# Kernel optimization log

Measured on AMD Instinct MI355X. Metric: run time of the kernel, lower is better.

## Reference

```python
import jax, jax.numpy as jnp
import numpy as np

B = 1024
M = 131072          # memory_size
K = 256             # key_dim
CHOOSE_K = 256
BETA = 1e-08
EPS = 0.001


def setup_inputs() -> dict:
    key = jax.random.key(0)
    k1, k2, k3 = jax.random.split(key, 3)
    q = jax.random.normal(k1, (B, K), dtype=jnp.float32)
    mk = jax.random.normal(k2, (M, K), dtype=jnp.float32)
    memory_key = mk / jnp.linalg.norm(mk, axis=1, keepdims=True)  # unit-norm keys as in update_memory
    # __init__: first half values = 1 (real), second half = 0 (fake)
    memory_values = jnp.concatenate([jnp.ones((M // 2,), jnp.float32),
                                     jnp.zeros((M - M // 2,), jnp.float32)])
    # hist starts near 1e-5; add small positive noise so p_c is non-degenerate
    memory_hist = 1e-05 + 1e-05 * jax.random.uniform(k3, (M,), dtype=jnp.float32)
    return {"q": q, "memory_key": memory_key,
            "memory_values": memory_values, "memory_hist": memory_hist}


def reference(q, memory_key, memory_values, memory_hist):
    # similarities: [B, M]
    similarities = jnp.matmul(q, memory_key.T)
    p_x_given_c_unnorm = jnp.exp(similarities)
    hist_b = memory_hist + BETA
    p_c = hist_b / jnp.sum(hist_b)                       # [M]
    p_c_given_x = p_x_given_c_unnorm * p_c               # [B, M]
    p_c_given_x_approx, idxs = jax.lax.top_k(p_c_given_x, CHOOSE_K)  # [B, k]
    vals = memory_values[idxs]                           # gather, [B, k]
    p_y_given_x_unnorm = jnp.sum(vals * p_c_given_x_approx, axis=1)
    p_y_given_x = p_y_given_x_unnorm / jnp.sum(p_c_given_x_approx, axis=1)
    return jnp.clip(p_y_given_x, EPS, 1.0 - EPS)
```

## Files before the change

kernel.cpp:

```cpp
#include <hip/hip_runtime.h>
#include <math.h>
#include <stdint.h>

#define MMEM 131072
#define KDIM 256
#define NB   1024
#define TOPK 256
#define BETA_F 1e-08f
#define NTILE 2048
#define OVFCAP 65536
#define SLOTS 4
#define SBINS 1024
#define SCAP  2560
#define SBCAP 256

typedef _Float16 f16x8 __attribute__((ext_vector_type(8)));
typedef float    f32x4 __attribute__((ext_vector_type(4)));

__device__ __forceinline__ void gload16(const void* g, void* l) {
  __builtin_amdgcn_global_load_lds(
      (const __attribute__((address_space(1))) uint32_t*)g,
      (__attribute__((address_space(3))) uint32_t*)l, 16, 0, 0);
}

#define NQ4 (NB * KDIM / 4)
#define NM4 (MMEM * KDIM / 4)
#define CVTB ((NQ4 + NM4) / 256)
__global__ __launch_bounds__(256) void prep_kernel(const float* __restrict__ q,
                                                   const float* __restrict__ mk,
                                                   _Float16* __restrict__ qh,
                                                   _Float16* __restrict__ mkh,
                                                   const float* __restrict__ hist,
                                                   float* __restrict__ partials,
                                                   float* __restrict__ partials_log) {
  const int b = blockIdx.x;
  if (b < CVTB) {
    int i = b * 256 + threadIdx.x;
    const float* in; _Float16* out; int j;
    if (i < NQ4) { in = q; out = qh; j = i; }
    else         { in = mk; out = mkh; j = i - NQ4; }
    float4 v = *(const float4*)&in[(size_t)j * 4];
    union { _Float16 h[4]; uint2 u; } p;
    p.h[0] = (_Float16)v.x; p.h[1] = (_Float16)v.y;
    p.h[2] = (_Float16)v.z; p.h[3] = (_Float16)v.w;
    *(uint2*)&out[(size_t)j * 4] = p.u;
    return;
  }
  const int bid = b - CVTB;
  float s = 0.f, sl = 0.f;
  for (int i = bid * 256 + threadIdx.x; i < MMEM; i += 256 * 256) {
    float h = hist[i] + BETA_F;
    s += h;
    sl += logf(h);
  }
  #pragma unroll
  for (int off = 32; off > 0; off >>= 1) {
    s  += __shfl_down(s, off);
    sl += __shfl_down(sl, off);
  }
  __shared__ float ws[4], wsl[4];
  int lane = threadIdx.x & 63, wid = threadIdx.x >> 6;
  if (lane == 0) { ws[wid] = s; wsl[wid] = sl; }
  __syncthreads();
  if (threadIdx.x == 0) {
    partials[bid]     = ws[0] + ws[1] + ws[2] + ws[3];
    partials_log[bid] = wsl[0] + wsl[1] + wsl[2] + wsl[3];
  }
}

__global__ __launch_bounds__(256) void logpc_final_kernel(const float* __restrict__ hist,
                                                          const float* __restrict__ partials,
                                                          const float* __restrict__ partials_log,
                                                          float* __restrict__ logpc,
                                                          float* __restrict__ out_sum,
                                                          float* __restrict__ out_thresh,
                                                          uint32_t* __restrict__ ovf_cnt,
                                                          float z0) {
  __shared__ float ws[4], wsl[4];
  const int tid = threadIdx.x;
  float s = partials[tid];
  float sl = (blockIdx.x == 0) ? partials_log[tid] : 0.f;
  #pragma unroll
  for (int off = 32; off > 0; off >>= 1) {
    s  += __shfl_down(s, off);
    sl += __shfl_down(sl, off);
  }
  int lane = tid & 63, wid = tid >> 6;
  if (lane == 0) { ws[wid] = s; wsl[wid] = sl; }
  __syncthreads();
  const float sum = ws[0] + ws[1] + ws[2] + ws[3];
  const int i = blockIdx.x * 256 + tid;
  logpc[i] = logf(hist[i] + BETA_F) - logf(sum);
  if (blockIdx.x == 0 && tid == 0) {
    float suml = wsl[0] + wsl[1] + wsl[2] + wsl[3];
    *out_sum = sum;
    *out_thresh = suml / (float)MMEM - logf(sum) + z0;
    *ovf_cnt = 0u;
  }
}

__global__ __launch_bounds__(256, 3) void gemm_kernel(const _Float16* __restrict__ qh,
                                                      const _Float16* __restrict__ mkh,
                                                      const float* __restrict__ logpc,
                                                      const float* __restrict__ values,
                                                      const float* __restrict__ thresh,
                                                      float2* __restrict__ cand,
                                                      uint8_t* __restrict__ cnt,
                                                      int4* __restrict__ ovf,
                                                      uint32_t* __restrict__ ovf_cnt) {
  __shared__ _Float16 As[3][4096];
  __shared__ _Float16 Bs[3][4096];

  const int t    = threadIdx.x;
  const int lane = t & 63;
  const int wave = t >> 6;
  const int wr   = (wave & 1) * 64;
  const int wc   = (wave >> 1) * 64;
  const int lm   = lane & 15;
  const int lk   = lane >> 4;

  const int wg  = blockIdx.x;
  const int lg  = ((wg & 7) << 10) | (wg >> 3);
  const int row0 = (lg & 7) << 7;
  const int col0 = (lg >> 3) << 7;

  const int r0q = t >> 2;
  const int cc  = (t & 3) ^ ((r0q >> 1) & 3);

  const char* gA0 = (const char*)qh  + ((size_t)(row0 + r0q)      * KDIM) * 2 + cc * 16;
  const char* gA1 = (const char*)qh  + ((size_t)(row0 + 64 + r0q) * KDIM) * 2 + cc * 16;
  const char* gB0 = (const char*)mkh + ((size_t)(col0 + r0q)      * KDIM) * 2 + cc * 16;
  const char* gB1 = (const char*)mkh + ((size_t)(col0 + 64 + r0q) * KDIM) * 2 + cc * 16;

  int offA[4], offB[4];
  #pragma unroll
  for (int i = 0; i < 4; ++i) {
    int ar = wr + i * 16 + lm;
    offA[i] = ar * 64 + ((lk ^ ((ar >> 1) & 3)) * 16);
    int br = wc + i * 16 + lm;
    offB[i] = br * 64 + ((lk ^ ((br >> 1) & 3)) * 16);
  }

  const float tv = *thresh;
  float lpv[4], vv[4];
  #pragma unroll
  for (int j = 0; j < 4; ++j) {
    lpv[j] = logpc[col0 + wc + j * 16 + lm];
    vv[j]  = values[col0 + wc + j * 16 + lm];
  }
  asm volatile("s_waitcnt vmcnt(0)" ::: "memory");

  f32x4 acc[4][4];
  #pragma unroll
  for (int i = 0; i < 4; i++)
    #pragma unroll
    for (int j = 0; j < 4; j++)
      acc[i][j] = (f32x4){0.f, 0.f, 0.f, 0.f};

  auto stage = [&](int buf, int chunk) {
    const size_t ko = (size_t)chunk * 64;
    gload16(gA0 + ko, (char*)&As[buf][0] + t * 16);
    gload16(gA1 + ko, (char*)&As[buf][0] + 4096 + t * 16);
    gload16(gB0 + ko, (char*)&Bs[buf][0] + t * 16);
    gload16(gB1 + ko, (char*)&Bs[buf][0] + 4096 + t * 16);
  };

  stage(0, 0);
  stage(1, 1);
  asm volatile("s_waitcnt vmcnt(4)" ::: "memory");
  __builtin_amdgcn_s_barrier();
  asm volatile("" ::: "memory");

  #pragma unroll
  for (int it = 0; it < 8; ++it) {
    const int cur = it % 3;
    const char* Ab = (const char*)&As[cur][0];
    const char* Bb = (const char*)&Bs[cur][0];
    f16x8 af[4], bf[4];
    #pragma unroll
    for (int i = 0; i < 4; ++i) af[i] = *(const f16x8*)(Ab + offA[i]);
    #pragma unroll
    for (int j = 0; j < 4; ++j) bf[j] = *(const f16x8*)(Bb + offB[j]);
    if (it + 2 < 8) stage((it + 2) % 3, it + 2);
    __builtin_amdgcn_s_setprio(1);
    #pragma unroll
    for (int i = 0; i < 4; ++i)
      #pragma unroll
      for (int j = 0; j < 4; ++j)
        acc[i][j] = __builtin_amdgcn_mfma_f32_16x16x32_f16(af[i], bf[j], acc[i][j], 0, 0, 0);
    __builtin_amdgcn_s_setprio(0);
    if (it < 7) {
      if (it + 2 < 8) asm volatile("s_waitcnt vmcnt(4)" ::: "memory");
      else            asm volatile("s_waitcnt vmcnt(0)" ::: "memory");
      __builtin_amdgcn_s_barrier();
      asm volatile("" ::: "memory");
    }
  }

  const int coltile = (col0 + wc) >> 6;
  const uint32_t ltm = (1u << lm) - 1u;
  const int shift = lane & 48;
  #pragma unroll
  for (int i = 0; i < 4; ++i) {
    #pragma unroll
    for (int r4 = 0; r4 < 4; ++r4) {
      const int row = row0 + wr + i * 16 + lk * 4 + r4;
      float sv[4];
      uint32_t gm[4];
      int tot = 0;
      #pragma unroll
      for (int j = 0; j < 4; ++j) {
        sv[j] = acc[i][j][r4] + lpv[j];
        gm[j] = (uint32_t)((__ballot(sv[j] >= tv) >> shift) & 0xFFFFull);
        tot += __popc(gm[j]);
      }
      const size_t bucket = (size_t)row * NTILE + coltile;
      if (lm == 0) cnt[bucket] = (uint8_t)(tot < SLOTS ? tot : SLOTS);
      float2* bs = cand + bucket * SLOTS;
      int prev = 0;
      #pragma unroll
      for (int j = 0; j < 4; ++j) {
        if ((gm[j] >> lm) & 1u) {
          int k = prev + __popc(gm[j] & ltm);
          if (k < SLOTS) {
            bs[k] = make_float2(sv[j], vv[j]);
          } else {
            int col = col0 + wc + j * 16 + lm;
            uint32_t p = atomicAdd(ovf_cnt, 1u);
            if (p < OVFCAP) ovf[p] = make_int4(row, col, __float_as_int(sv[j]),
                                               __float_as_int(vv[j]));
          }
        }
        prev += __popc(gm[j]);
      }
    }
  }
}

__global__ __launch_bounds__(512) void select_kernel(const float2* __restrict__ cand,
                                                     const uint8_t* __restrict__ cnt,
                                                     const int4* __restrict__ ovf,
                                                     const uint32_t* __restrict__ ovf_cnt,
                                                     const float* __restrict__ thresh,
                                                     float* __restrict__ out) {
  __shared__ uint32_t hist[SBINS];
  __shared__ float cs_s[SCAP];
  __shared__ float cs_v[SCAP];
  __shared__ uint32_t csum[32];
  __shared__ int s_bstar, s_above, s_ccnt, s_bcnt;
  __shared__ float bin_s[SBCAP];
  __shared__ float bin_v[SBCAP];
  __shared__ float red_p[8], red_vp[8];

  const int tid = threadIdx.x;
  const int row = blockIdx.x;
  const float tv = *thresh;
  const int novf = (int)min(*ovf_cnt, (uint32_t)OVFCAP);

  for (int i = tid; i < SBINS; i += 512) hist[i] = 0;
  if (tid == 0) { s_ccnt = 0; s_bcnt = 0; }
  __syncthreads();

  for (int tile = tid; tile < NTILE; tile += 512) {
    size_t bucket = (size_t)row * NTILE + tile;
    int c = (int)cnt[bucket];
    if (c > 0) {
      const float4* b4 = (const float4*)(cand + bucket * SLOTS);
      float4 lo = b4[0];
      float4 hi = b4[1];
      float sc0 = lo.x, vl0 = lo.y, sc1 = lo.z, vl1 = lo.w;
      float sc2 = hi.x, vl2 = hi.y, sc3 = hi.z, vl3 = hi.w;
      #pragma unroll
      for (int k = 0; k < 4; k++) {
        if (k < c) {
          float s = (k == 0) ? sc0 : (k == 1) ? sc1 : (k == 2) ? sc2 : sc3;
          float v = (k == 0) ? vl0 : (k == 1) ? vl1 : (k == 2) ? vl2 : vl3;
          int b = (int)((s - tv) * 256.0f);
          b = b < 0 ? 0 : (b > SBINS - 1 ? SBINS - 1 : b);
          atomicAdd(&hist[b], 1u);
          int pos = atomicAdd(&s_ccnt, 1);
          if (pos < SCAP) { cs_s[pos] = s; cs_v[pos] = v; }
        }
      }
    }
  }
  for (int i = tid; i < novf; i += 512) {
    int4 e = ovf[i];
    if (e.x == row) {
      float s = __int_as_float(e.z);
      float v = __int_as_float(e.w);
      int b = (int)((s - tv) * 256.0f);
      b = b < 0 ? 0 : (b > SBINS - 1 ? SBINS - 1 : b);
      atomicAdd(&hist[b], 1u);
      int pos = atomicAdd(&s_ccnt, 1);
      if (pos < SCAP) { cs_s[pos] = s; cs_v[pos] = v; }
    }
  }
  __syncthreads();

  if (tid < 32) {
    uint32_t s = 0;
    for (int b = 0; b < 32; b++) s += hist[tid * 32 + b];
    csum[tid] = s;
  }
  __syncthreads();
  if (tid == 0) {
    uint32_t cum = 0;
    int bstar = 0; uint32_t above = 0;
    for (int c = 31; c >= 0; c--) {
      if (cum + csum[c] >= TOPK) {
        for (int b = 31; b >= 0; b--) {
          uint32_t h = hist[c * 32 + b];
          if (cum + h >= TOPK) { bstar = c * 32 + b; above = cum; goto found; }
          cum += h;
        }
      }
      cum += csum[c];
    }
    bstar = 0; above = cum - hist[0];
  found:
    s_bstar = bstar;
    s_above = (int)above;
  }
  __syncthreads();
  const int bstar = s_bstar;
  int rneed = TOPK - s_above;
  const int ctot = s_ccnt;

  float psum = 0.f, vpsum = 0.f;
  if (ctot <= SCAP) {
    for (int i = tid; i < ctot; i += 512) {
      float s = cs_s[i];
      float v = cs_v[i];
      int b = (int)((s - tv) * 256.0f);
      b = b < 0 ? 0 : (b > SBINS - 1 ? SBINS - 1 : b);
      if (b > bstar) {
        float p = __expf(s);
        psum += p;
        vpsum += p * v;
      } else if (b == bstar) {
        int pos = atomicAdd(&s_bcnt, 1);
        if (pos < SBCAP) { bin_s[pos] = s; bin_v[pos] = v; }
      }
    }
  } else {
    for (int tile = tid; tile < NTILE; tile += 512) {
      size_t bucket = (size_t)row * NTILE + tile;
      int c = (int)cnt[bucket];
      const float2* bs = cand + bucket * SLOTS;
      for (int k = 0; k < c; k++) {
        float2 e = bs[k];
        int b = (int)((e.x - tv) * 256.0f);
        b = b < 0 ? 0 : (b > SBINS - 1 ? SBINS - 1 : b);
        if (b > bstar) {
          float p = __expf(e.x);
          psum += p;
          vpsum += p * e.y;
        } else if (b == bstar) {
          int pos = atomicAdd(&s_bcnt, 1);
          if (pos < SBCAP) { bin_s[pos] = e.x; bin_v[pos] = e.y; }
        }
      }
    }
    for (int i = tid; i < novf; i += 512) {
      int4 e = ovf[i];
      if (e.x == row) {
        float s = __int_as_float(e.z);
        float v = __int_as_float(e.w);
        int b = (int)((s - tv) * 256.0f);
        b = b < 0 ? 0 : (b > SBINS - 1 ? SBINS - 1 : b);
        if (b > bstar) {
          float p = __expf(s);
          psum += p;
          vpsum += p * v;
        } else if (b == bstar) {
          int pos = atomicAdd(&s_bcnt, 1);
          if (pos < SBCAP) { bin_s[pos] = s; bin_v[pos] = v; }
        }
      }
    }
  }
  __syncthreads();

  int c2 = s_bcnt < SBCAP ? s_bcnt : SBCAP;
  int n2 = 1;
  while (n2 < c2) n2 <<= 1;
  for (int i = c2 + tid; i < n2; i += 512) { bin_s[i] = -INFINITY; bin_v[i] = 0.f; }
  __syncthreads();

  for (int size = 2; size <= n2; size <<= 1) {
    for (int stride = size >> 1; stride > 0; stride >>= 1) {
      for (int i = tid; i < n2; i += 512) {
        int j = i ^ stride;
        if (j > i) {
          float si = bin_s[i], sj = bin_s[j];
          float vi = bin_v[i], vj = bin_v[j];
          bool igt = (si > sj) || (si == sj && vi > vj);
          bool desc = ((i & size) == 0);
          if (desc ? !igt : igt) {
            bin_s[i] = sj; bin_s[j] = si;
            bin_v[i] = vj; bin_v[j] = vi;
          }
        }
      }
      __syncthreads();
    }
  }

  int take = rneed < c2 ? rneed : c2;
  if (take < 0) take = 0;
  for (int i = tid; i < take; i += 512) {
    float p = __expf(bin_s[i]);
    psum += p;
    vpsum += p * bin_v[i];
  }

  #pragma unroll
  for (int off = 32; off > 0; off >>= 1) {
    psum  += __shfl_down(psum, off);
    vpsum += __shfl_down(vpsum, off);
  }
  int lane = tid & 63, wid = tid >> 6;
  if (lane == 0) { red_p[wid] = psum; red_vp[wid] = vpsum; }
  __syncthreads();
  if (tid == 0) {
    float P = 0.f, V = 0.f;
    for (int w = 0; w < 8; w++) { P += red_p[w]; V += red_vp[w]; }
    float r = V / P;
    r = fminf(fmaxf(r, 1e-3f), 1.0f - 1e-3f);
    out[row] = r;
  }
}

extern "C" void kernel_launch(void* const* d_in, const int* in_sizes, int n_in,
                              void* d_out, int out_size, void* d_ws, size_t ws_size,
                              hipStream_t stream) {
  const float* q      = (const float*)d_in[0];
  const float* mk     = (const float*)d_in[1];
  const float* values = (const float*)d_in[2];
  const float* hist   = (const float*)d_in[3];
  float* out = (float*)d_out;

  float*    ws_sum   = (float*)d_ws;
  float*    ws_thr   = (float*)((char*)d_ws + 64);
  uint32_t* ovf_cnt  = (uint32_t*)((char*)d_ws + 128);
  float*    partials = (float*)((char*)d_ws + 4096);
  float*    partialsl= (float*)((char*)d_ws + 8192);
  float*    logpc    = (float*)((char*)d_ws + 16384);
  _Float16* qh       = (_Float16*)((char*)d_ws + 540672);
  _Float16* mkh      = (_Float16*)((char*)d_ws + 1064960);
  uint8_t*  cnt      = (uint8_t*)((char*)d_ws + 68173824ull);
  int4*     ovf      = (int4*)((char*)d_ws + 76562432ull);
  float2*   cand     = (float2*)((char*)d_ws + 77611008ull);

  const float z0 = 2.4176f;

  prep_kernel<<<CVTB + 256, 256, 0, stream>>>(q, mk, qh, mkh, hist, partials, partialsl);
  logpc_final_kernel<<<MMEM / 256, 256, 0, stream>>>(hist, partials, partialsl, logpc,
                                                     ws_sum, ws_thr, ovf_cnt, z0);
  gemm_kernel<<<(NB / 128) * (MMEM / 128), 256, 0, stream>>>(
      qh, mkh, logpc, values, ws_thr, cand, cnt, ovf, ovf_cnt);
  select_kernel<<<NB, 512, 0, stream>>>(cand, cnt, ovf, ovf_cnt, ws_thr, out);
}
```

Measured before the change: 340.3 us.

## Widen fp16 conversion, skip empty bucket writes, scan counts by word, split GEMM launch

The fp16 conversion in prep now has each thread handle 16 floats with 128-bit stores instead of 4 floats per thread. In the GEMM epilogue, lanes skip the candidate-store loop when a bucket has no hits. The select kernel reads the per-tile counts four bytes at a time and skips all-zero words. The GEMM launch is also split into two half-grid launches using a workgroup offset, which adds one launch but leaves total work the same.

```diff
diff --git a/kernel.cpp b/kernel.cpp
--- a/kernel.cpp
+++ b/kernel.cpp
@@ -23,9 +23,9 @@
       (__attribute__((address_space(3))) uint32_t*)l, 16, 0, 0);
 }
 
-#define NQ4 (NB * KDIM / 4)
-#define NM4 (MMEM * KDIM / 4)
-#define CVTB ((NQ4 + NM4) / 256)
+#define NQ16 (NB * KDIM / 16)
+#define NM16 (MMEM * KDIM / 16)
+#define CVTB ((NQ16 + NM16) / 256)
 __global__ __launch_bounds__(256) void prep_kernel(const float* __restrict__ q,
                                                    const float* __restrict__ mk,
                                                    _Float16* __restrict__ qh,
@@ -36,14 +36,20 @@
   const int b = blockIdx.x;
   if (b < CVTB) {
     int i = b * 256 + threadIdx.x;
-    const float* in; _Float16* out; int j;
-    if (i < NQ4) { in = q; out = qh; j = i; }
-    else         { in = mk; out = mkh; j = i - NQ4; }
-    float4 v = *(const float4*)&in[(size_t)j * 4];
-    union { _Float16 h[4]; uint2 u; } p;
-    p.h[0] = (_Float16)v.x; p.h[1] = (_Float16)v.y;
-    p.h[2] = (_Float16)v.z; p.h[3] = (_Float16)v.w;
-    *(uint2*)&out[(size_t)j * 4] = p.u;
+    const float* in; _Float16* out; size_t j;
+    if (i < NQ16) { in = q;  out = qh;  j = (size_t)i; }
+    else          { in = mk; out = mkh; j = (size_t)(i - NQ16); }
+    const float4* src = (const float4*)(in + j * 16);
+    union { _Float16 h[16]; uint4 u[2]; } p;
+    #pragma unroll
+    for (int k = 0; k < 4; ++k) {
+      float4 v = src[k];
+      p.h[k * 4 + 0] = (_Float16)v.x; p.h[k * 4 + 1] = (_Float16)v.y;
+      p.h[k * 4 + 2] = (_Float16)v.z; p.h[k * 4 + 3] = (_Float16)v.w;
+    }
+    uint4* dst = (uint4*)(out + j * 16);
+    dst[0] = p.u[0];
+    dst[1] = p.u[1];
     return;
   }
   const int bid = b - CVTB;
@@ -107,7 +113,8 @@
                                                       float2* __restrict__ cand,
                                                       uint8_t* __restrict__ cnt,
                                                       int4* __restrict__ ovf,
-                                                      uint32_t* __restrict__ ovf_cnt) {
+                                                      uint32_t* __restrict__ ovf_cnt,
+                                                      int wgoff) {
   __shared__ _Float16 As[3][4096];
   __shared__ _Float16 Bs[3][4096];
 
@@ -119,7 +126,7 @@
   const int lm   = lane & 15;
   const int lk   = lane >> 4;
 
-  const int wg  = blockIdx.x;
+  const int wg  = blockIdx.x + wgoff;
   const int lg  = ((wg & 7) << 10) | (wg >> 3);
   const int row0 = (lg & 7) << 7;
   const int col0 = (lg >> 3) << 7;
@@ -216,22 +223,24 @@
       }
       const size_t bucket = (size_t)row * NTILE + coltile;
       if (lm == 0) cnt[bucket] = (uint8_t)(tot < SLOTS ? tot : SLOTS);
-      float2* bs = cand + bucket * SLOTS;
-      int prev = 0;
-      #pragma unroll
-      for (int j = 0; j < 4; ++j) {
-        if ((gm[j] >> lm) & 1u) {
-          int k = prev + __popc(gm[j] & ltm);
-          if (k < SLOTS) {
-            bs[k] = make_float2(sv[j], vv[j]);
-          } else {
-            int col = col0 + wc + j * 16 + lm;
-            uint32_t p = atomicAdd(ovf_cnt, 1u);
-            if (p < OVFCAP) ovf[p] = make_int4(row, col, __float_as_int(sv[j]),
-                                               __float_as_int(vv[j]));
+      if (tot) {
+        float2* bs = cand + bucket * SLOTS;
+        int prev = 0;
+        #pragma unroll
+        for (int j = 0; j < 4; ++j) {
+          if ((gm[j] >> lm) & 1u) {
+            int k = prev + __popc(gm[j] & ltm);
+            if (k < SLOTS) {
+              bs[k] = make_float2(sv[j], vv[j]);
+            } else {
+              int col = col0 + wc + j * 16 + lm;
+              uint32_t p = atomicAdd(ovf_cnt, 1u);
+              if (p < OVFCAP) ovf[p] = make_int4(row, col, __float_as_int(sv[j]),
+                                                 __float_as_int(vv[j]));
+            }
           }
-        }
-        prev += __popc(gm[j]);
+          prev += __popc(gm[j]);
+        }
       }
     }
   }
@@ -261,25 +270,31 @@
   if (tid == 0) { s_ccnt = 0; s_bcnt = 0; }
   __syncthreads();
 
-  for (int tile = tid; tile < NTILE; tile += 512) {
-    size_t bucket = (size_t)row * NTILE + tile;
-    int c = (int)cnt[bucket];
-    if (c > 0) {
-      const float4* b4 = (const float4*)(cand + bucket * SLOTS);
-      float4 lo = b4[0];
-      float4 hi = b4[1];
-      float sc0 = lo.x, vl0 = lo.y, sc1 = lo.z, vl1 = lo.w;
-      float sc2 = hi.x, vl2 = hi.y, sc3 = hi.z, vl3 = hi.w;
+  {
+    const uint32_t* cnt32 = (const uint32_t*)(cnt + (size_t)row * NTILE);
+    for (int w = tid; w < NTILE / 4; w += 512) {
+      uint32_t cw = cnt32[w];
+      if (cw == 0u) continue;
       #pragma unroll
-      for (int k = 0; k < 4; k++) {
-        if (k < c) {
-          float s = (k == 0) ? sc0 : (k == 1) ? sc1 : (k == 2) ? sc2 : sc3;
-          float v = (k == 0) ? vl0 : (k == 1) ? vl1 : (k == 2) ? vl2 : vl3;
-          int b = (int)((s - tv) * 256.0f);
-          b = b < 0 ? 0 : (b > SBINS - 1 ? SBINS - 1 : b);
-          atomicAdd(&hist[b], 1u);
-          int pos = atomicAdd(&s_ccnt, 1);
-          if (pos < SCAP) { cs_s[pos] = s; cs_v[pos] = v; }
+      for (int s4 = 0; s4 < 4; ++s4) {
+        int c = (int)((cw >> (8 * s4)) & 0xFFu);
+        if (c > 0) {
+          size_t bucket = (size_t)row * NTILE + (w * 4 + s4);
+          const float4* b4 = (const float4*)(cand + bucket * SLOTS);
+          float4 lo = b4[0];
+          float4 hi = b4[1];
+          #pragma unroll
+          for (int k = 0; k < 4; k++) {
+            if (k < c) {
+              float s = (k == 0) ? lo.x : (k == 1) ? lo.z : (k == 2) ? hi.x : hi.z;
+              float v = (k == 0) ? lo.y : (k == 1) ? lo.w : (k == 2) ? hi.y : hi.w;
+              int b = (int)((s - tv) * 256.0f);
+              b = b < 0 ? 0 : (b > SBINS - 1 ? SBINS - 1 : b);
+              atomicAdd(&hist[b], 1u);
+              int pos = atomicAdd(&s_ccnt, 1);
+              if (pos < SCAP) { cs_s[pos] = s; cs_v[pos] = v; }
+            }
+          }
         }
       }
     }
@@ -458,7 +473,9 @@
   prep_kernel<<<CVTB + 256, 256, 0, stream>>>(q, mk, qh, mkh, hist, partials, partialsl);
   logpc_final_kernel<<<MMEM / 256, 256, 0, stream>>>(hist, partials, partialsl, logpc,
                                                      ws_sum, ws_thr, ovf_cnt, z0);
-  gemm_kernel<<<(NB / 128) * (MMEM / 128), 256, 0, stream>>>(
-      qh, mkh, logpc, values, ws_thr, cand, cnt, ovf, ovf_cnt);
+  gemm_kernel<<<4096, 256, 0, stream>>>(qh, mkh, logpc, values, ws_thr,
+                                        cand, cnt, ovf, ovf_cnt, 0);
+  gemm_kernel<<<4096, 256, 0, stream>>>(qh, mkh, logpc, values, ws_thr,
+                                        cand, cnt, ovf, ovf_cnt, 4096);
   select_kernel<<<NB, 512, 0, stream>>>(cand, cnt, ovf, ovf_cnt, ws_thr, out);
 }
```

New measurement: 359.3 us. 5.6% more time.
